# Kernel optimization log

Hardware: AMD Instinct MI355X
Metric: run time of the kernel (lower is better)

Reference implementation:

```python
import jax, jax.numpy as jnp
import numpy as np

B = 262144
D = 128          # d_model
DFF = 4 * D      # 512, FFN expansion
T = 16           # num_tiles
TPC = 4          # tiles_per_cluster
NC = T // TPC    # 4 clusters
NOPS = 8         # len(OPCODES)
EMB = 32
FEAT = EMB + 17  # 49
TW, SW, DW = 0.01, 0.005, 0.01  # ternary / sparsity / diversity weights


def ternary_quant(W):
    # per-tile ternary quantization: threshold at 0.7 * mean|W|, scale = mean|W|
    s0 = jnp.mean(jnp.abs(W))
    return s0 * jnp.sign(W) * (jnp.abs(W) > 0.7 * s0).astype(W.dtype)


def setup_inputs() -> dict:
    key = jax.random.key(0)
    ks = jax.random.split(key, 16)
    inp = {
        'op_idx': jax.random.randint(ks[0], (B,), 0, NOPS),
        'a': jax.random.randint(ks[1], (B,), 0, 256),
        'b': jax.random.randint(ks[2], (B,), 0, 256),
        'c': jax.random.randint(ks[3], (B,), 0, 2),
        # parameters
        'op_embed': jax.random.normal(ks[4], (NOPS, EMB), jnp.float32),
        'W_in': jax.random.normal(ks[5], (FEAT, D), jnp.float32) / np.sqrt(FEAT),
        'b_in': jnp.zeros((D,), jnp.float32),
        'Wr': jax.random.normal(ks[6], (D, T), jnp.float32) / np.sqrt(D),
        'W1': jax.random.normal(ks[7], (T, D, DFF), jnp.float32) / np.sqrt(D),
        'W2': jax.random.normal(ks[8], (T, DFF, D), jnp.float32) / np.sqrt(DFF),
        'Wh1': jax.random.normal(ks[9], (D, 64), jnp.float32) / np.sqrt(D),
        'bh1': jnp.zeros((64,), jnp.float32),
        'Wh2': jax.random.normal(ks[10], (64, 8), jnp.float32) / np.sqrt(64),
        'bh2': jnp.zeros((8,), jnp.float32),
    }
    return inp


def reference(op_embed, W_in, b_in, Wr, W1, W2, Wh1, bh1, Wh2, bh2, op_idx, a, b, c):
    bits = lambda v: ((v[:, None] >> jnp.arange(8)) & 1).astype(jnp.float32)  # [B,8]
    emb = op_embed[op_idx]  # [B,32]
    x = jnp.concatenate([emb, bits(a), bits(b), c[:, None].astype(jnp.float32)], axis=1)  # [B,49]
    x = x @ W_in + b_in  # [B,D]

    # tile routing (top-1)
    logits = x @ Wr                      # [B,T]
    probs = jax.nn.softmax(logits, -1)
    idx = jnp.argmax(probs, -1)          # [B]
    gate = jnp.max(probs, -1)            # [B]

    # ternary-quantized per-tile FFN weights
    W1q = jax.vmap(ternary_quant)(W1)    # [T,D,DFF]
    W2q = jax.vmap(ternary_quant)(W2)    # [T,DFF,D]

    out = jnp.zeros_like(x)
    for t in range(T):  # fixed small tile set
        y = jax.nn.gelu(x @ W1q[t]) @ W2q[t]          # [B,D]
        out = out + jnp.where((idx == t)[:, None], y, 0.0)
    out = out * gate[:, None]

    # aux losses
    one_hot = jax.nn.one_hot(idx, T, dtype=x.dtype)
    frac = one_hot.mean(0)               # tokens per tile
    meanp = probs.mean(0)                # mean router prob per tile
    sparsity = T * jnp.sum(frac * meanp)              # load-balance (Switch-style)
    tern = jnp.mean(jnp.abs(W1 - W1q)) + jnp.mean(jnp.abs(W2 - W2q))
    cp = meanp.reshape(NC, TPC).sum(-1)               # cluster usage
    diversity = jnp.sum(cp * jnp.log(cp + 1e-9))      # negative entropy
    aux = TW * tern + SW * sparsity + DW * diversity

    h = jax.nn.relu(out @ Wh1 + bh1)
    result = jax.nn.sigmoid(h @ Wh2 + bh2)  # [B,8]
    return result, idx, aux
```

## Files before the change

kernel.cpp:

```cpp
#include <hip/hip_runtime.h>
#include <hip/hip_bf16.h>
#include <math.h>

typedef __attribute__((ext_vector_type(8))) short short8;
typedef __attribute__((ext_vector_type(4))) float floatx4;
typedef __attribute__((ext_vector_type(4))) unsigned int uintx4;
typedef __attribute__((ext_vector_type(2))) unsigned int uintx2;

__device__ __forceinline__ unsigned short f2bf(float f) {
    unsigned int u = __float_as_uint(f);
    unsigned int r = (u + 0x7fffu + ((u >> 16) & 1u)) >> 16;
    return (unsigned short)r;
}

__device__ __forceinline__ unsigned int cvtpk(float a, float b) {
    unsigned int r;
    asm("v_cvt_pk_bf16_f32 %0, %1, %2" : "=v"(r) : "v"(a), "v"(b));
    return r;
}

__device__ __forceinline__ void permlane32_swap(unsigned int &a, unsigned int &b) {
    asm volatile("v_permlane32_swap_b32 %0, %1" : "+v"(a), "+v"(b));
}
__device__ __forceinline__ void permlane16_swap(unsigned int &a, unsigned int &b) {
    asm volatile("v_permlane16_swap_b32 %0, %1" : "+v"(a), "+v"(b));
}

__device__ __forceinline__ float gelu_f(float u) {
    float u2 = u * u;
    float p = __builtin_fmaf(u2, -0.102943242f, -2.302208184f);
    float z = p * u;
    float e;
    asm("v_exp_f32 %0, %1" : "=v"(e) : "v"(z));
    return u * __builtin_amdgcn_rcpf(1.0f + e);
}

__device__ __forceinline__ floatx4 mfma16(short8 a, short8 b, floatx4 c) {
    return __builtin_amdgcn_mfma_f32_16x16x32_bf16(a, b, c, 0, 0, 0);
}


__global__ __launch_bounds__(256) void k_sumabs(const float* __restrict__ W1,
                                                const float* __restrict__ W2,
                                                float* __restrict__ partials) {
    int blk = blockIdx.x;
    bool isW1 = blk < 256;
    const float* W = (isW1 ? W1 : W2) + (long)(isW1 ? blk : blk - 256) * 4096;
    float s = 0.f;
    #pragma unroll
    for (int i = 0; i < 4; i++) {
        floatx4 v = *(const floatx4*)(W + i * 1024 + threadIdx.x * 4);
        s += fabsf(v[0]) + fabsf(v[1]) + fabsf(v[2]) + fabsf(v[3]);
    }
    __shared__ float red[256];
    red[threadIdx.x] = s; __syncthreads();
    for (int st = 128; st > 0; st >>= 1) {
        if (threadIdx.x < st) red[threadIdx.x] += red[threadIdx.x + st];
        __syncthreads();
    }
    if (threadIdx.x == 0) partials[blk] = red[0];
}

__global__ __launch_bounds__(256) void k_quant(
        const float* __restrict__ W1, const float* __restrict__ W2,
        const float* __restrict__ partials,
        unsigned short* __restrict__ W1qT, unsigned short* __restrict__ W2qT,
        float* ternsum) {
    int blk = blockIdx.x;
    bool isW1 = blk < 256;
    long el0 = (long)(isW1 ? blk : blk - 256) * 4096;
    int t = (int)(el0 >> 16);
    const float* part = partials + (isW1 ? 0 : 256) + t * 16;
    float ssum = 0.f;
    #pragma unroll
    for (int i = 0; i < 16; i++) ssum += part[i];
    float s = ssum * (1.0f / 65536.0f);
    float thr = 0.7f * s;
    unsigned int us = (unsigned int)f2bf(s);
    const float* Wsrc = (isW1 ? W1 : W2) + el0;
    unsigned short* dst = (isW1 ? W1qT : W2qT) + (long)t * 65536;
    int locbase = (int)(el0 & 65535);
    float dsum = 0.f;
    #pragma unroll
    for (int i = 0; i < 4; i++) {
        int off = i * 1024 + threadIdx.x * 4;
        floatx4 w = *(const floatx4*)(Wsrc + off);
        int loc = locbase + off;
        #pragma unroll
        for (int r = 0; r < 4; r++) {
            float wv = w[r];
            float aw = fabsf(wv);
            bool big = aw > thr;
            dsum += big ? fabsf(aw - s) : aw;
            unsigned int sign15 = (__float_as_uint(wv) >> 16) & 0x8000u;
            unsigned short q = big ? (unsigned short)(us | sign15) : (unsigned short)0;
            int lr = loc + r;
            int addr = isW1 ? ((lr & 511) * 128 + (lr >> 9))
                            : ((lr & 127) * 512 + (lr >> 7));
            dst[addr] = q;
        }
    }
    __shared__ float red[256];
    red[threadIdx.x] = dsum; __syncthreads();
    for (int st2 = 128; st2 > 0; st2 >>= 1) {
        if (threadIdx.x < st2) red[threadIdx.x] += red[threadIdx.x + st2];
        __syncthreads();
    }
    if (threadIdx.x == 0) atomicAdd(ternsum, red[0]);
}

__global__ __launch_bounds__(256) void k_w23(
        const unsigned short* __restrict__ W2qT, const float* __restrict__ Wh1,
        unsigned short* __restrict__ W23qT) {
    int t = blockIdx.x >> 6, h = blockIdx.x & 63;
    __shared__ float wcol[128];
    if (threadIdx.x < 128) wcol[threadIdx.x] = Wh1[threadIdx.x * 64 + h];
    __syncthreads();
    int k2 = threadIdx.x * 2;
    const unsigned short* w2 = W2qT + (long)t * 65536 + k2;
    float a0 = 0.f, a1 = 0.f;
    #pragma unroll 8
    for (int d = 0; d < 128; d++) {
        unsigned int u = *(const unsigned int*)(w2 + d * 512);
        float w = wcol[d];
        a0 += w * __uint_as_float(u << 16);
        a1 += w * __uint_as_float(u & 0xffff0000u);
    }
    *(unsigned int*)(W23qT + ((long)(t * 64 + h)) * 512 + k2) = cvtpk(a0, a1);
}

__global__ void k_tables(const float* __restrict__ op_embed, const float* __restrict__ W_in,
                         const float* __restrict__ b_in,
                         float* embW, float* Ta, float* Tb, float* Tc) {
    int i = blockIdx.x * 256 + threadIdx.x;
    if (i < 1024) {
        int op = i >> 7, j = i & 127;
        float s = b_in[j];
        #pragma unroll
        for (int k = 0; k < 32; k++) s += op_embed[op * 32 + k] * W_in[k * 128 + j];
        embW[i] = s;
    } else if (i < 1024 + 32768) {
        int r = i - 1024; int a = r >> 7, j = r & 127;
        float s = 0.f;
        #pragma unroll
        for (int bit = 0; bit < 8; bit++) if ((a >> bit) & 1) s += W_in[(32 + bit) * 128 + j];
        Ta[r] = s;
    } else if (i < 33792 + 32768) {
        int r = i - 33792; int b = r >> 7, j = r & 127;
        float s = 0.f;
        #pragma unroll
        for (int bit = 0; bit < 8; bit++) if ((b >> bit) & 1) s += W_in[(40 + bit) * 128 + j];
        Tb[r] = s;
    } else if (i < 66560 + 128) {
        int j = i - 66560; Tc[j] = W_in[48 * 128 + j];
    }
}

__global__ void k_tablesR(const float* __restrict__ embW, const float* __restrict__ Ta,
                          const float* __restrict__ Tb, const float* __restrict__ Tc,
                          const float* __restrict__ Wr,
                          float* embWr, float* TaR, float* TbR, float* TcR) {
    int i = blockIdx.x * 256 + threadIdx.x;
    int row = i >> 4, t = i & 15;
    const float* src; float* dst;
    if (row < 8)        { src = embW + row * 128;        dst = embWr + i; }
    else if (row < 264) { src = Ta + (row - 8) * 128;    dst = TaR + (row - 8) * 16 + t; }
    else if (row < 520) { src = Tb + (row - 264) * 128;  dst = TbR + (row - 264) * 16 + t; }
    else if (row == 520){ src = Tc;                      dst = TcR + t; }
    else return;
    float s = 0.f;
    for (int j = 0; j < 128; j++) s += src[j] * Wr[j * 16 + t];
    *dst = s;
}


__global__ __launch_bounds__(256) void k_front(
        const int* __restrict__ op_idx, const int* __restrict__ a_in,
        const int* __restrict__ b_in_i, const int* __restrict__ c_in,
        const float* __restrict__ embW, const float* __restrict__ Ta,
        const float* __restrict__ Tb, const float* __restrict__ Tc,
        const float* __restrict__ embWr, const float* __restrict__ TaR,
        const float* __restrict__ TbR, const float* __restrict__ TcR,
        unsigned short* __restrict__ xq, float* __restrict__ gate_out,
        float* psum, int* cnt, float* __restrict__ d_idx) {
    __shared__ float sp[4][16];
    __shared__ int sc[4][16];
    int gid = blockIdx.x * 256 + threadIdx.x;
    int lane = threadIdx.x & 63;
    int j = lane & 15;
    int grpbase = lane & 48;
    float psum_acc = 0.f; int cnt_acc = 0;

    #pragma unroll 1
    for (int it = 0; it < 16; it++) {
        int tok = it * 16384 + (gid >> 4);
        int op = op_idx[tok], a = a_in[tok], b = b_in_i[tok], c = c_in[tok];
        float cf = (float)c;

        float lg = embWr[op * 16 + j] + TaR[a * 16 + j] + TbR[b * 16 + j] + cf * TcR[j];
        float m = lg;
        m = fmaxf(m, __shfl_xor(m, 8, 16));
        m = fmaxf(m, __shfl_xor(m, 4, 16));
        m = fmaxf(m, __shfl_xor(m, 2, 16));
        m = fmaxf(m, __shfl_xor(m, 1, 16));
        float p = __expf(lg - m);
        float s = p;
        s += __shfl_xor(s, 8, 16);
        s += __shfl_xor(s, 4, 16);
        s += __shfl_xor(s, 2, 16);
        s += __shfl_xor(s, 1, 16);
        float g = __builtin_amdgcn_rcpf(s);
        unsigned long long ball = __ballot(lg == m);
        int bi = __ffsll((unsigned long long)((ball >> grpbase) & 0xffffULL)) - 1;
        psum_acc += p * g;
        cnt_acc += (j == bi) ? 1 : 0;
        if (j == 0) { gate_out[tok] = g; d_idx[tok] = (float)bi; }

        int d0 = j * 8;
        const floatx4* E  = (const floatx4*)(embW + op * 128 + d0);
        const floatx4* A4 = (const floatx4*)(Ta + a * 128 + d0);
        const floatx4* B4 = (const floatx4*)(Tb + b * 128 + d0);
        const floatx4* C4 = (const floatx4*)(Tc + d0);
        floatx4 v0 = E[0] + A4[0] + B4[0] + cf * C4[0];
        floatx4 v1 = E[1] + A4[1] + B4[1] + cf * C4[1];
        uintx4 o;
        o[0] = cvtpk(v0[0], v0[1]);
        o[1] = cvtpk(v0[2], v0[3]);
        o[2] = cvtpk(v1[0], v1[1]);
        o[3] = cvtpk(v1[2], v1[3]);
        *(uintx4*)(xq + (long)tok * 128 + d0) = o;
    }

    psum_acc += __shfl_xor(psum_acc, 16);
    psum_acc += __shfl_xor(psum_acc, 32);
    cnt_acc += __shfl_xor(cnt_acc, 16);
    cnt_acc += __shfl_xor(cnt_acc, 32);
    int wv = threadIdx.x >> 6;
    if (lane < 16) { sp[wv][j] = psum_acc; sc[wv][j] = cnt_acc; }
    __syncthreads();
    if (threadIdx.x < 16) {
        int jj = threadIdx.x;
        atomicAdd(&psum[jj], sp[0][jj] + sp[1][jj] + sp[2][jj] + sp[3][jj]);
        atomicAdd(&cnt[jj], sc[0][jj] + sc[1][jj] + sc[2][jj] + sc[3][jj]);
    }
}


__global__ void k_scatter(const float* __restrict__ d_idx, const int* __restrict__ cnt,
                          int* fill, int* __restrict__ bucket) {
    __shared__ int lc[16], lbase[16];
    if (threadIdx.x < 16) lc[threadIdx.x] = 0;
    __syncthreads();
    int offs[16];
    {
        int off = 0;
        #pragma unroll
        for (int tt = 0; tt < 16; tt++) { offs[tt] = off; off += cnt[tt]; }
    }
    int tok = blockIdx.x * 256 + threadIdx.x;
    int t = (int)d_idx[tok];
    int lpos = atomicAdd(&lc[t], 1);
    __syncthreads();
    if (threadIdx.x < 16) lbase[threadIdx.x] = atomicAdd(&fill[threadIdx.x], lc[threadIdx.x]);
    __syncthreads();
    bucket[offs[t] + lbase[t] + lpos] = tok;
}


__global__ __launch_bounds__(256, 3) void k_ffn(
    const unsigned short* __restrict__ xq, const float* __restrict__ gate,
    const int* __restrict__ bucket, const int* __restrict__ cnt_g,
    const float* __restrict__ psum_g, const float* __restrict__ ternsum_g,
    const unsigned short* __restrict__ W1qT, const unsigned short* __restrict__ W23qT,
    const float* __restrict__ Wh2, const float* __restrict__ bh1,
    const float* __restrict__ bh2,
    float* __restrict__ result, float* __restrict__ d_aux) {

    extern __shared__ __align__(16) unsigned char smem[];
    unsigned short* Ax = (unsigned short*)smem;
    float* Red = (float*)(smem + 17408);
    int*   toks = (int*)(smem + 50176);
    float* gats = (float*)(smem + 50432);
    float* Wh2l = (float*)(smem + 50688);
    float* bh2l = (float*)(smem + 52736);
    float* bh1l = (float*)(smem + 52768);

    int bid = blockIdx.x;
    int t = -1, ci = 0, nt = 0, base = 0;
    {
        int coff = 0, off = 0;
        #pragma unroll 1
        for (int tt = 0; tt < 16; tt++) {
            int c = cnt_g[tt];
            int ch = (c + 63) >> 6;
            if (t < 0 && bid < coff + ch) { t = tt; ci = bid - coff; nt = c; base = off + ci * 64; }
            coff += ch; off += c;
        }
    }
    if (t < 0) return;
    int nvalid = nt - ci * 64; if (nvalid > 64) nvalid = 64;

    int tid = threadIdx.x;
    if (tid < 64) {
        int tk = (tid < nvalid) ? bucket[base + tid] : -1;
        toks[tid] = tk;
        gats[tid] = (tk >= 0) ? gate[tk] : 0.0f;
    }
    Wh2l[tid] = Wh2[tid];
    Wh2l[tid + 256] = Wh2[tid + 256];
    if (tid < 8) bh2l[tid] = bh2[tid];
    else if (tid < 72) bh1l[tid - 8] = bh1[tid - 8];
    __syncthreads();

    #pragma unroll
    for (int it = 0; it < 4; it++) {
        int seg = it * 256 + tid; int r = seg >> 4, sg = seg & 15;
        int tk = toks[r];
        uintx4 v = {0u, 0u, 0u, 0u};
        if (tk >= 0) v = *(const uintx4*)(xq + (long)tk * 128 + sg * 8);
        *(uintx4*)(Ax + r * 136 + sg * 8) = v;
    }
    __syncthreads();

    int lane = tid & 63, dh = tid >> 6;
    int lane15 = lane & 15, lgrp = lane >> 4;

    floatx4 acc3[4][4];
    #pragma unroll
    for (int i = 0; i < 4; i++)
        #pragma unroll
        for (int j = 0; j < 4; j++) acc3[i][j] = (floatx4){0.f, 0.f, 0.f, 0.f};

    const unsigned short* w1p  = W1qT + (long)t * 65536 + (dh * 32 + lane15) * 128 + lgrp * 8;
    const unsigned short* w23p = W23qT + ((long)t * 64 + lane15) * 512 + dh * 32 + lgrp * 8;

    for (int nc = 0; nc < 4; nc++) {
        floatx4 acc1[2][4];
        #pragma unroll
        for (int i = 0; i < 2; i++)
            #pragma unroll
            for (int j = 0; j < 4; j++) acc1[i][j] = (floatx4){0.f, 0.f, 0.f, 0.f};

        const unsigned short* w1c = w1p + nc * 16384;
        #pragma unroll
        for (int kk = 0; kk < 4; kk++) {
            short8 af0 = *(const short8*)(w1c + kk * 32);
            short8 af1 = *(const short8*)(w1c + 2048 + kk * 32);
            int ko = kk * 32 + lgrp * 8;
            #pragma unroll
            for (int mt = 0; mt < 4; mt++) {
                short8 bf = *(const short8*)(Ax + (mt * 16 + lane15) * 136 + ko);
                acc1[0][mt] = mfma16(af0, bf, acc1[0][mt]);
                acc1[1][mt] = mfma16(af1, bf, acc1[1][mt]);
            }
        }

        const unsigned short* w23c = w23p + nc * 128;
        short8 af23_0 = *(const short8*)(w23c);
        short8 af23_1 = *(const short8*)(w23c + 8192);
        short8 af23_2 = *(const short8*)(w23c + 16384);
        short8 af23_3 = *(const short8*)(w23c + 24576);

        #pragma unroll
        for (int mt = 0; mt < 4; mt++) {
            floatx4 v0 = acc1[0][mt], v1 = acc1[1][mt];
            unsigned int X0 = cvtpk(gelu_f(v0[0]), gelu_f(v0[1]));
            unsigned int X1 = cvtpk(gelu_f(v0[2]), gelu_f(v0[3]));
            unsigned int Y0 = cvtpk(gelu_f(v1[0]), gelu_f(v1[1]));
            unsigned int Y1 = cvtpk(gelu_f(v1[2]), gelu_f(v1[3]));
            permlane32_swap(X0, Y0);
            permlane16_swap(X0, Y0);
            permlane32_swap(X1, Y1);
            permlane16_swap(X1, Y1);
            union { uintx4 u; short8 s; } bu;
            bu.u[0] = X0; bu.u[1] = X1; bu.u[2] = Y0; bu.u[3] = Y1;
            short8 bfrag = bu.s;
            acc3[0][mt] = mfma16(af23_0, bfrag, acc3[0][mt]);
            acc3[1][mt] = mfma16(af23_1, bfrag, acc3[1][mt]);
            acc3[2][mt] = mfma16(af23_2, bfrag, acc3[2][mt]);
            acc3[3][mt] = mfma16(af23_3, bfrag, acc3[3][mt]);
        }
    }

    bool hi = (dh & 2) != 0;
    floatx4 k0[4], k1[4];
    {
        float* mybuf = Red + dh * 2048;
        #pragma unroll
        for (int mt = 0; mt < 4; mt++) {
            floatx4 s0 = hi ? acc3[0][mt] : acc3[2][mt];
            floatx4 s1 = hi ? acc3[1][mt] : acc3[3][mt];
            *(floatx4*)(mybuf + ((0 * 4 + mt) * 64 + lane) * 4) = s0;
            *(floatx4*)(mybuf + ((1 * 4 + mt) * 64 + lane) * 4) = s1;
            k0[mt] = hi ? acc3[2][mt] : acc3[0][mt];
            k1[mt] = hi ? acc3[3][mt] : acc3[1][mt];
        }
        __syncthreads();
        const float* pbuf = Red + (dh ^ 2) * 2048;
        #pragma unroll
        for (int mt = 0; mt < 4; mt++) {
            k0[mt] += *(const floatx4*)(pbuf + ((0 * 4 + mt) * 64 + lane) * 4);
            k1[mt] += *(const floatx4*)(pbuf + ((1 * 4 + mt) * 64 + lane) * 4);
        }
    }
    __syncthreads();
    bool lo1 = (dh & 1) != 0;
    floatx4 fin[4];
    {
        float* mybuf = Red + dh * 1024;
        #pragma unroll
        for (int mt = 0; mt < 4; mt++) {
            floatx4 sm = lo1 ? k0[mt] : k1[mt];
            *(floatx4*)(mybuf + (mt * 64 + lane) * 4) = sm;
            fin[mt] = lo1 ? k1[mt] : k0[mt];
        }
        __syncthreads();
        const float* pbuf = Red + (dh ^ 1) * 1024;
        #pragma unroll
        for (int mt = 0; mt < 4; mt++)
            fin[mt] += *(const floatx4*)(pbuf + (mt * 64 + lane) * 4);
    }
    __syncthreads();

    float* H = Red;
    int hb = dh * 16 + lgrp * 4;
    floatx4 b4 = *(const floatx4*)(bh1l + hb);
    #pragma unroll
    for (int mt = 0; mt < 4; mt++) {
        int m = mt * 16 + lane15;
        float gm = gats[m];
        floatx4 v;
        v[0] = fmaxf(fin[mt][0] * gm + b4[0], 0.f);
        v[1] = fmaxf(fin[mt][1] * gm + b4[1], 0.f);
        v[2] = fmaxf(fin[mt][2] * gm + b4[2], 0.f);
        v[3] = fmaxf(fin[mt][3] * gm + b4[3], 0.f);
        *(floatx4*)(H + m * 68 + hb) = v;
    }
    __syncthreads();

    int mloc = tid >> 2, c0 = (tid & 3) * 2;
    int tk = toks[mloc];
    float z0 = bh2l[c0], z1 = bh2l[c0 + 1];
    const floatx4* Hr4 = (const floatx4*)(H + mloc * 68);
    #pragma unroll
    for (int h4 = 0; h4 < 16; h4++) {
        floatx4 hv = Hr4[h4];
        #pragma unroll
        for (int r = 0; r < 4; r++) {
            int h = h4 * 4 + r;
            z0 += hv[r] * Wh2l[h * 8 + c0];
            z1 += hv[r] * Wh2l[h * 8 + c0 + 1];
        }
    }
    if (tk >= 0) {
        float2 rr;
        rr.x = __builtin_amdgcn_rcpf(1.0f + __expf(-z0));
        rr.y = __builtin_amdgcn_rcpf(1.0f + __expf(-z1));
        *(float2*)(result + (long)tk * 8 + c0) = rr;
    }

    if (bid == 0 && tid == 0) {
        const float Bf = 262144.0f;
        float tern = ternsum_g[0] * (1.0f / 1048576.0f);
        float sp = 0.f; float cp[4] = {0.f, 0.f, 0.f, 0.f};
        for (int tt = 0; tt < 16; tt++) {
            float frac = (float)cnt_g[tt] / Bf, mp = psum_g[tt] / Bf;
            sp += frac * mp; cp[tt >> 2] += mp;
        }
        float dv = 0.f;
        for (int cc = 0; cc < 4; cc++) dv += cp[cc] * logf(cp[cc] + 1e-9f);
        d_aux[0] = 0.01f * tern + 0.005f * (16.0f * sp) + 0.01f * dv;
    }
}


extern "C" void kernel_launch(void* const* d_in, const int* in_sizes, int n_in,
                              void* d_out, int out_size, void* d_ws, size_t ws_size,
                              hipStream_t stream) {
    const int* op_idx = (const int*)d_in[0];
    const int* a_in   = (const int*)d_in[1];
    const int* b_in_i = (const int*)d_in[2];
    const int* c_in   = (const int*)d_in[3];
    const float* op_embed = (const float*)d_in[4];
    const float* W_in  = (const float*)d_in[5];
    const float* b_in  = (const float*)d_in[6];
    const float* Wr    = (const float*)d_in[7];
    const float* W1    = (const float*)d_in[8];
    const float* W2    = (const float*)d_in[9];
    const float* Wh1   = (const float*)d_in[10];
    const float* bh1   = (const float*)d_in[11];
    const float* Wh2   = (const float*)d_in[12];
    const float* bh2   = (const float*)d_in[13];

    const long B = in_sizes[0];
    float* result = (float*)d_out;
    float* d_idx  = (float*)d_out + B * 8;
    float* d_aux  = (float*)d_out + B * 9;

    unsigned char* ws = (unsigned char*)d_ws;
    unsigned short* xq    = (unsigned short*)(ws + 0);
    unsigned short* W1qT  = (unsigned short*)(ws + 67108864);
    unsigned short* W2qT  = (unsigned short*)(ws + 69206016);
    unsigned short* W23qT = (unsigned short*)(ws + 71303168);
    float* gate  = (float*)(ws + 72351744);
    int*   bucket= (int*)  (ws + 73400320);
    float* Ta    = (float*)(ws + 74448896);
    float* Tb    = (float*)(ws + 74579968);
    float* embW  = (float*)(ws + 74711040);
    float* Tc    = (float*)(ws + 74715136);
    float* TaR   = (float*)(ws + 74715648);
    float* TbR   = (float*)(ws + 74732032);
    float* embWr = (float*)(ws + 74748416);
    float* TcR   = (float*)(ws + 74748928);
    float* partials = (float*)(ws + 74748992);
    unsigned char* acc = ws + 74751040;
    float* ternsum = (float*)(acc + 0);
    float* psum    = (float*)(acc + 64);
    int*   cnt     = (int*)(acc + 128);
    int*   fill    = (int*)(acc + 192);

    hipMemsetAsync(acc, 0, 256, stream);

    k_sumabs<<<512, 256, 0, stream>>>(W1, W2, partials);
    k_quant<<<512, 256, 0, stream>>>(W1, W2, partials, W1qT, W2qT, ternsum);
    k_tables<<<261, 256, 0, stream>>>(op_embed, W_in, b_in, embW, Ta, Tb, Tc);
    k_tablesR<<<33, 256, 0, stream>>>(embW, Ta, Tb, Tc, Wr, embWr, TaR, TbR, TcR);
    k_front<<<1024, 256, 0, stream>>>(op_idx, a_in, b_in_i, c_in,
                                      embW, Ta, Tb, Tc, embWr, TaR, TbR, TcR,
                                      xq, gate, psum, cnt, d_idx);
    k_w23<<<1024, 256, 0, stream>>>(W2qT, Wh1, W23qT);
    k_scatter<<<(int)(B / 256), 256, 0, stream>>>(d_idx, cnt, fill, bucket);
    k_ffn<<<4112, 256, 53024, stream>>>(xq, gate, bucket, cnt, psum, ternsum,
                                        W1qT, W23qT, Wh2, bh1, bh2, result, d_aux);
}
```

Measured before the change: 279.4 us.

## Stage quantized transpose in LDS and shrink FFN reduction scratch for occupancy

The quantization kernel now writes transposed ternary weights into shared memory and then stores them to global memory with coalesced 16-byte writes, replacing the scattered 2-byte global stores. The FFN kernel's cross-wave reduction becomes a rotated ring of three exchange steps over a single 4 KB slot per wave, which halves the Red scratch. Shared memory per block drops from about 53 KB to about 36.6 KB, and launch bounds move to 4 blocks per CU. The W23 fragment loads are rotated per wave to line up with that ring. The costs are more barriers in the epilogue and a tighter register budget, which risks spills.

Result: slower. 315.6 us (+12.9%).

```diff
diff --git a/kernel.cpp b/kernel.cpp
--- a/kernel.cpp
+++ b/kernel.cpp
@@ -66,10 +66,12 @@
         const float* __restrict__ partials,
         unsigned short* __restrict__ W1qT, unsigned short* __restrict__ W2qT,
         float* ternsum) {
+    __shared__ unsigned short Lq[4096];
+    __shared__ float red[256];
     int blk = blockIdx.x;
     bool isW1 = blk < 256;
-    long el0 = (long)(isW1 ? blk : blk - 256) * 4096;
-    int t = (int)(el0 >> 16);
+    int rb = isW1 ? blk : blk - 256;
+    int t = rb >> 4, slab = rb & 15;
     const float* part = partials + (isW1 ? 0 : 256) + t * 16;
     float ssum = 0.f;
     #pragma unroll
@@ -77,36 +79,60 @@
     float s = ssum * (1.0f / 65536.0f);
     float thr = 0.7f * s;
     unsigned int us = (unsigned int)f2bf(s);
-    const float* Wsrc = (isW1 ? W1 : W2) + el0;
-    unsigned short* dst = (isW1 ? W1qT : W2qT) + (long)t * 65536;
-    int locbase = (int)(el0 & 65535);
+    int tid = threadIdx.x;
     float dsum = 0.f;
-    #pragma unroll
-    for (int i = 0; i < 4; i++) {
-        int off = i * 1024 + threadIdx.x * 4;
-        floatx4 w = *(const floatx4*)(Wsrc + off);
-        int loc = locbase + off;
-        #pragma unroll
-        for (int r = 0; r < 4; r++) {
-            float wv = w[r];
-            float aw = fabsf(wv);
-            bool big = aw > thr;
-            dsum += big ? fabsf(aw - s) : aw;
-            unsigned int sign15 = (__float_as_uint(wv) >> 16) & 0x8000u;
-            unsigned short q = big ? (unsigned short)(us | sign15) : (unsigned short)0;
-            int lr = loc + r;
-            int addr = isW1 ? ((lr & 511) * 128 + (lr >> 9))
-                            : ((lr & 127) * 512 + (lr >> 7));
-            dst[addr] = q;
-        }
-    }
-    __shared__ float red[256];
-    red[threadIdx.x] = dsum; __syncthreads();
+    if (isW1) {
+        int f0 = slab * 32;
+        int d = tid >> 1, fh = (tid & 1) * 16;
+        const float* src = W1 + (long)t * 65536 + d * 512 + f0 + fh;
+        #pragma unroll
+        for (int i = 0; i < 4; i++) {
+            floatx4 w = *(const floatx4*)(src + i * 4);
+            #pragma unroll
+            for (int r = 0; r < 4; r++) {
+                float wv = w[r];
+                float aw = fabsf(wv);
+                bool big = aw > thr;
+                dsum += big ? fabsf(aw - s) : aw;
+                unsigned int sign15 = (__float_as_uint(wv) >> 16) & 0x8000u;
+                unsigned short q = big ? (unsigned short)(us | sign15) : (unsigned short)0;
+                Lq[(fh + i * 4 + r) * 128 + d] = q;
+            }
+        }
+    } else {
+        int d0 = slab * 8;
+        int f = tid * 2;
+        const float* src = W2 + (long)t * 65536 + f * 128 + d0;
+        #pragma unroll
+        for (int rr = 0; rr < 2; rr++) {
+            #pragma unroll
+            for (int i = 0; i < 2; i++) {
+                floatx4 w = *(const floatx4*)(src + rr * 128 + i * 4);
+                #pragma unroll
+                for (int r = 0; r < 4; r++) {
+                    float wv = w[r];
+                    float aw = fabsf(wv);
+                    bool big = aw > thr;
+                    dsum += big ? fabsf(aw - s) : aw;
+                    unsigned int sign15 = (__float_as_uint(wv) >> 16) & 0x8000u;
+                    unsigned short q = big ? (unsigned short)(us | sign15) : (unsigned short)0;
+                    Lq[(i * 4 + r) * 512 + f + rr] = q;
+                }
+            }
+        }
+    }
+    __syncthreads();
+    unsigned short* dst = (isW1 ? W1qT : W2qT) + (long)t * 65536 + slab * 4096;
+    const uintx4* Ls = (const uintx4*)Lq;
+    uintx4* D4 = (uintx4*)dst;
+    D4[tid] = Ls[tid];
+    D4[tid + 256] = Ls[tid + 256];
+    red[tid] = dsum; __syncthreads();
     for (int st2 = 128; st2 > 0; st2 >>= 1) {
-        if (threadIdx.x < st2) red[threadIdx.x] += red[threadIdx.x + st2];
+        if (tid < st2) red[tid] += red[tid + st2];
         __syncthreads();
     }
-    if (threadIdx.x == 0) atomicAdd(ternsum, red[0]);
+    if (tid == 0) atomicAdd(ternsum, red[0]);
 }
 
 __global__ __launch_bounds__(256) void k_w23(
@@ -267,7 +293,7 @@
 }
 
 
-__global__ __launch_bounds__(256, 3) void k_ffn(
+__global__ __launch_bounds__(256, 4) void k_ffn(
     const unsigned short* __restrict__ xq, const float* __restrict__ gate,
     const int* __restrict__ bucket, const int* __restrict__ cnt_g,
     const float* __restrict__ psum_g, const float* __restrict__ ternsum_g,
@@ -279,11 +305,11 @@
     extern __shared__ __align__(16) unsigned char smem[];
     unsigned short* Ax = (unsigned short*)smem;
     float* Red = (float*)(smem + 17408);
-    int*   toks = (int*)(smem + 50176);
-    float* gats = (float*)(smem + 50432);
-    float* Wh2l = (float*)(smem + 50688);
-    float* bh2l = (float*)(smem + 52736);
-    float* bh1l = (float*)(smem + 52768);
+    int*   toks = (int*)(smem + 33792);
+    float* gats = (float*)(smem + 34048);
+    float* Wh2l = (float*)(smem + 34304);
+    float* bh2l = (float*)(smem + 36352);
+    float* bh1l = (float*)(smem + 36384);
 
     int bid = blockIdx.x;
     int t = -1, ci = 0, nt = 0, base = 0;
@@ -332,7 +358,11 @@
         for (int j = 0; j < 4; j++) acc3[i][j] = (floatx4){0.f, 0.f, 0.f, 0.f};
 
     const unsigned short* w1p  = W1qT + (long)t * 65536 + (dh * 32 + lane15) * 128 + lgrp * 8;
-    const unsigned short* w23p = W23qT + ((long)t * 64 + lane15) * 512 + dh * 32 + lgrp * 8;
+    const unsigned short* w23p = W23qT + (long)t * 32768 + lane15 * 512 + dh * 32 + lgrp * 8;
+    int ho0 = dh * 8192;
+    int ho1 = ((dh + 1) & 3) * 8192;
+    int ho2 = ((dh + 2) & 3) * 8192;
+    int ho3 = ((dh + 3) & 3) * 8192;
 
     for (int nc = 0; nc < 4; nc++) {
         floatx4 acc1[2][4];
@@ -356,10 +386,10 @@
         }
 
         const unsigned short* w23c = w23p + nc * 128;
-        short8 af23_0 = *(const short8*)(w23c);
-        short8 af23_1 = *(const short8*)(w23c + 8192);
-        short8 af23_2 = *(const short8*)(w23c + 16384);
-        short8 af23_3 = *(const short8*)(w23c + 24576);
+        short8 af23_0 = *(const short8*)(w23c + ho0);
+        short8 af23_1 = *(const short8*)(w23c + ho1);
+        short8 af23_2 = *(const short8*)(w23c + ho2);
+        short8 af23_3 = *(const short8*)(w23c + ho3);
 
         #pragma unroll
         for (int mt = 0; mt < 4; mt++) {
@@ -382,47 +412,45 @@
         }
     }
 
-    bool hi = (dh & 2) != 0;
-    floatx4 k0[4], k1[4];
+    floatx4 fin[4];
+    #pragma unroll
+    for (int mt = 0; mt < 4; mt++) fin[mt] = acc3[0][mt];
+    float* myslot = Red + dh * 1024;
+    int lofs = lane * 4;
+    #pragma unroll
+    for (int mt = 0; mt < 4; mt++)
+        *(floatx4*)(myslot + mt * 256 + lofs) = acc3[1][mt];
+    __syncthreads();
     {
-        float* mybuf = Red + dh * 2048;
-        #pragma unroll
-        for (int mt = 0; mt < 4; mt++) {
-            floatx4 s0 = hi ? acc3[0][mt] : acc3[2][mt];
-            floatx4 s1 = hi ? acc3[1][mt] : acc3[3][mt];
-            *(floatx4*)(mybuf + ((0 * 4 + mt) * 64 + lane) * 4) = s0;
-            *(floatx4*)(mybuf + ((1 * 4 + mt) * 64 + lane) * 4) = s1;
-            k0[mt] = hi ? acc3[2][mt] : acc3[0][mt];
-            k1[mt] = hi ? acc3[3][mt] : acc3[1][mt];
-        }
-        __syncthreads();
-        const float* pbuf = Red + (dh ^ 2) * 2048;
-        #pragma unroll
-        for (int mt = 0; mt < 4; mt++) {
-            k0[mt] += *(const floatx4*)(pbuf + ((0 * 4 + mt) * 64 + lane) * 4);
-            k1[mt] += *(const floatx4*)(pbuf + ((1 * 4 + mt) * 64 + lane) * 4);
-        }
-    }
-    __syncthreads();
-    bool lo1 = (dh & 1) != 0;
-    floatx4 fin[4];
+        const float* ps = Red + ((dh + 3) & 3) * 1024;
+        #pragma unroll
+        for (int mt = 0; mt < 4; mt++)
+            fin[mt] += *(const floatx4*)(ps + mt * 256 + lofs);
+    }
+    __syncthreads();
+    #pragma unroll
+    for (int mt = 0; mt < 4; mt++)
+        *(floatx4*)(myslot + mt * 256 + lofs) = acc3[2][mt];
+    __syncthreads();
     {
-        float* mybuf = Red + dh * 1024;
-        #pragma unroll
-        for (int mt = 0; mt < 4; mt++) {
-            floatx4 sm = lo1 ? k0[mt] : k1[mt];
-            *(floatx4*)(mybuf + (mt * 64 + lane) * 4) = sm;
-            fin[mt] = lo1 ? k1[mt] : k0[mt];
-        }
-        __syncthreads();
-        const float* pbuf = Red + (dh ^ 1) * 1024;
+        const float* ps = Red + ((dh + 2) & 3) * 1024;
         #pragma unroll
         for (int mt = 0; mt < 4; mt++)
-            fin[mt] += *(const floatx4*)(pbuf + (mt * 64 + lane) * 4);
-    }
-    __syncthreads();
-
-    float* H = Red;
+            fin[mt] += *(const floatx4*)(ps + mt * 256 + lofs);
+    }
+    __syncthreads();
+    #pragma unroll
+    for (int mt = 0; mt < 4; mt++)
+        *(floatx4*)(myslot + mt * 256 + lofs) = acc3[3][mt];
+    __syncthreads();
+    {
+        const float* ps = Red + ((dh + 1) & 3) * 1024;
+        #pragma unroll
+        for (int mt = 0; mt < 4; mt++)
+            fin[mt] += *(const floatx4*)(ps + mt * 256 + lofs);
+    }
+
+    float* H = (float*)Ax;
     int hb = dh * 16 + lgrp * 4;
     floatx4 b4 = *(const floatx4*)(bh1l + hb);
     #pragma unroll
@@ -530,6 +558,6 @@
                                       xq, gate, psum, cnt, d_idx);
     k_w23<<<1024, 256, 0, stream>>>(W2qT, Wh1, W23qT);
     k_scatter<<<(int)(B / 256), 256, 0, stream>>>(d_idx, cnt, fill, bucket);
-    k_ffn<<<4112, 256, 53024, stream>>>(xq, gate, bucket, cnt, psum, ternsum,
+    k_ffn<<<4112, 256, 36640, stream>>>(xq, gate, bucket, cnt, psum, ternsum,
                                         W1qT, W23qT, Wh2, bh1, bh2, result, d_aux);
 }
```
